# Kernel tuning notes

Measured on AMD Instinct MI355X. Metric: run time of the kernel, lower is better.

Reference implementation:

```python
import jax, jax.numpy as jnp
import numpy as np

D_MODEL = 1024
N_HEADS = 16
DEPTH = D_MODEL // N_HEADS
DFF = 4096
B, S = 2, 2048
EPS = 1e-6


def layer_norm(x, gamma, beta):
    m = jnp.mean(x, axis=-1, keepdims=True)
    v = jnp.mean(jnp.square(x - m), axis=-1, keepdims=True)
    return (x - m) * jax.lax.rsqrt(v + EPS) * gamma + beta


def setup_inputs() -> dict:
    key = jax.random.key(0)
    ks = jax.random.split(key, 16)
    s = 0.02
    x = jax.random.normal(ks[0], (B, S, D_MODEL), dtype=jnp.float32)
    # causal mask: 1.0 where attention is NOT allowed (upper triangle)
    mask = (1.0 - jnp.tril(jnp.ones((S, S), dtype=jnp.float32)))[None, None, :, :]
    return {
        "x": x,
        "mask": mask,
        "wq": jax.random.normal(ks[1], (D_MODEL, D_MODEL), jnp.float32) * s,
        "bq": jnp.zeros((D_MODEL,), jnp.float32),
        "wk": jax.random.normal(ks[2], (D_MODEL, D_MODEL), jnp.float32) * s,
        "bk": jnp.zeros((D_MODEL,), jnp.float32),
        "wv": jax.random.normal(ks[3], (D_MODEL, D_MODEL), jnp.float32) * s,
        "bv": jnp.zeros((D_MODEL,), jnp.float32),
        "wo": jax.random.normal(ks[4], (D_MODEL, D_MODEL), jnp.float32) * s,
        "bo": jnp.zeros((D_MODEL,), jnp.float32),
        "g1": jnp.ones((D_MODEL,), jnp.float32),
        "be1": jnp.zeros((D_MODEL,), jnp.float32),
        "w1": jax.random.normal(ks[5], (D_MODEL, DFF), jnp.float32) * s,
        "b1": jnp.zeros((DFF,), jnp.float32),
        "w2": jax.random.normal(ks[6], (DFF, D_MODEL), jnp.float32) * s,
        "b2": jnp.zeros((D_MODEL,), jnp.float32),
        "g2": jnp.ones((D_MODEL,), jnp.float32),
        "be2": jnp.zeros((D_MODEL,), jnp.float32),
    }


def reference(x, mask, wq, bq, wk, bk, wv, bv, wo, bo, g1, be1, w1, b1, w2, b2, g2, be2):
    b, s = x.shape[0], x.shape[1]

    def heads(t):  # [B,S,D_MODEL] -> [B,H,S,depth]
        return t.reshape(b, s, N_HEADS, DEPTH).transpose(0, 2, 1, 3)

    q = heads(x @ wq + bq)
    k = heads(x @ wk + bk)
    v = heads(x @ wv + bv)

    # [B,H,S,S] scores, materialized as in the original
    logits = jnp.einsum("bhqd,bhkd->bhqk", q, k) / jnp.sqrt(jnp.float32(DEPTH))
    logits = logits + mask * (-1e9)
    attn = jax.nn.softmax(logits, axis=-1)
    ctx = jnp.einsum("bhqk,bhkd->bhqd", attn, v)
    ctx = ctx.transpose(0, 2, 1, 3).reshape(b, s, D_MODEL)
    attn_out = ctx @ wo + bo

    out1 = layer_norm(x + attn_out, g1, be1)
    ffn = jax.nn.relu(out1 @ w1 + b1) @ w2 + b2
    out2 = layer_norm(out1 + ffn, g2, be2)
    return out2  # dropout inactive (training=False)
```

## Files before the change

### kernel.cpp

```cpp
#include <hip/hip_runtime.h>
#include <stdint.h>

typedef unsigned short u16;
typedef unsigned int u32;
typedef __attribute__((ext_vector_type(8))) short short8;
typedef __attribute__((ext_vector_type(4))) float f32x4;

#define NHEADS 16
#define SEQ 2048
#define DM 1024
#define MROWS 4096
#define FF 4096

static_assert(sizeof(short8) == 16, "short8 must be 16B");

__device__ __forceinline__ u16 f2b(float f) {
  u32 u = __float_as_uint(f);
  u += 0x7fffu + ((u >> 16) & 1u);
  return (u16)(u >> 16);
}
__device__ __forceinline__ u32 f2b2(float lo, float hi) {
  u32 a = __float_as_uint(lo); a += 0x7fffu + ((a >> 16) & 1u);
  u32 b = __float_as_uint(hi); b += 0x7fffu + ((b >> 16) & 1u);
  return (a >> 16) | (b & 0xffff0000u);
}
__device__ __forceinline__ u32 f2b2t(float lo, float hi) {
  return __builtin_amdgcn_perm(__float_as_uint(hi), __float_as_uint(lo), 0x07060302u);
}
__device__ __forceinline__ float b2f(u16 h) { return __uint_as_float(((u32)h) << 16); }

__device__ __forceinline__ void async_cp16(const u16* g, u16* l) {
  __builtin_amdgcn_global_load_lds((const __attribute__((address_space(1))) void*)g,
                                   (__attribute__((address_space(3))) void*)l, 16, 0, 0);
}

__global__ __launch_bounds__(256) void prep_k(const float* __restrict__ x,
                                              const float* __restrict__ wq,
                                              const float* __restrict__ wk,
                                              const float* __restrict__ wv,
                                              const float* __restrict__ wo,
                                              const float* __restrict__ w1,
                                              const float* __restrict__ w2,
                                              u16* __restrict__ xb, u16* __restrict__ btq,
                                              u16* __restrict__ wot, u16* __restrict__ w1t,
                                              u16* __restrict__ w2t) {
  const int bid = blockIdx.x, tid = threadIdx.x;
  if (bid < 4096) {
    const int i = bid * 256 + tid;
    const float4 v = ((const float4*)x)[i];
    uint2 o; o.x = f2b2(v.x, v.y); o.y = f2b2(v.z, v.w);
    ((uint2*)xb)[i] = o;
    return;
  }
  __shared__ float tile[32][33];
  const int tb = bid - 4096;
  const float* in; u16* out; int N, K, n0, k0;
  if (tb < 4096) {
    const int m = tb >> 10, t = tb & 1023;
    if (m == 0) { in = wq; out = btq; }
    else if (m == 1) { in = wk; out = btq + 1024 * 1024; }
    else if (m == 2) { in = wv; out = btq + 2 * 1024 * 1024; }
    else { in = wo; out = wot; }
    N = 1024; K = 1024; n0 = (t & 31) * 32; k0 = (t >> 5) * 32;
  } else if (tb < 8192) {
    const int t = tb - 4096;
    in = w1; out = w1t; N = 4096; K = 1024; n0 = (t & 127) * 32; k0 = (t >> 7) * 32;
  } else {
    const int t = tb - 8192;
    in = w2; out = w2t; N = 1024; K = 4096; n0 = (t & 31) * 32; k0 = (t >> 5) * 32;
  }
  const int tx = tid & 31, ty = tid >> 5;
#pragma unroll
  for (int i = 0; i < 4; i++) {
    const int r = ty + i * 8;
    tile[r][tx] = in[(long)(k0 + r) * N + n0 + tx];
  }
  __syncthreads();
#pragma unroll
  for (int i = 0; i < 4; i++) {
    const int r = ty + i * 8;
    out[(long)(n0 + r) * K + k0 + tx] = f2b(tile[tx][r]);
  }
}

#define BM 128
#define BN 128
#define BK 64
#define EPI_QKV 0
#define EPI_ADDRES 1
#define EPI_RELUB 2

template <int EPI>
__global__ __launch_bounds__(256, 2) void gemm_bt(
    const u16* __restrict__ A, const u16* __restrict__ Bt, const int M, const int N,
    const int K, const float* __restrict__ bias0, const float* __restrict__ bias1,
    const float* __restrict__ bias2, const float* __restrict__ resid,
    float* __restrict__ outF, u16* __restrict__ outB, u16* __restrict__ outQ,
    u16* __restrict__ outK, u16* __restrict__ outV) {
  __shared__ u16 As[BM * BK];
  __shared__ u16 Bs[BN * BK];
  const int tid = threadIdx.x;
  const int lane = tid & 63;
  const int wv = tid >> 6;
  const int quad = lane >> 4;
  const int lm = lane & 15;
  const int tn = blockIdx.x * BN;
  const int tm = blockIdx.y * BM;
  const int wr = (wv >> 1) * 64;
  const int wc = (wv & 1) * 64;
  const int wslotbase = tid & ~63;

  const f32x4 z4 = {0.f, 0.f, 0.f, 0.f};
  f32x4 acc[4][4];
#pragma unroll
  for (int i = 0; i < 4; i++)
#pragma unroll
    for (int j = 0; j < 4; j++) acc[i][j] = z4;

  for (int kk = 0; kk < K; kk += BK) {
    __syncthreads();
#pragma unroll
    for (int t = 0; t < 4; t++) {
      const int slot = t * 256 + tid;
      const int row = slot >> 3;
      const int c = (slot & 7) ^ (row & 7);
      async_cp16(A + (long)(tm + row) * K + kk + c * 8,
                 As + (long)(t * 256 + wslotbase) * 8);
    }
#pragma unroll
    for (int t = 0; t < 4; t++) {
      const int slot = t * 256 + tid;
      const int row = slot >> 3;
      const int c = (slot & 7) ^ (row & 7);
      async_cp16(Bt + (long)(tn + row) * K + kk + c * 8,
                 Bs + (long)(t * 256 + wslotbase) * 8);
    }
    __syncthreads();
#pragma unroll
    for (int ks = 0; ks < 2; ks++) {
      short8 af[4], bf[4];
#pragma unroll
      for (int mi = 0; mi < 4; mi++) {
        const int row = wr + mi * 16 + lm;
        const int cc = (4 * ks + quad) ^ (row & 7);
        af[mi] = *(const short8*)(As + row * 64 + cc * 8);
      }
#pragma unroll
      for (int ni = 0; ni < 4; ni++) {
        const int row = wc + ni * 16 + lm;
        const int cc = (4 * ks + quad) ^ (row & 7);
        bf[ni] = *(const short8*)(Bs + row * 64 + cc * 8);
      }
#pragma unroll
      for (int mi = 0; mi < 4; mi++)
#pragma unroll
        for (int ni = 0; ni < 4; ni++)
          acc[mi][ni] =
              __builtin_amdgcn_mfma_f32_16x16x32_bf16(af[mi], bf[ni], acc[mi][ni], 0, 0, 0);
    }
  }

  if constexpr (EPI == EPI_QKV) {
    const int which = tn >> 10;
    const int bb = tm >> 11;
    if (which < 2) {
      const float* bs = which == 0 ? bias0 : bias1;
      u16* os = which == 0 ? outQ : outK;
      const float scale = which == 0 ? 0.125f * 1.44269504f : 1.0f;
#pragma unroll
      for (int ni = 0; ni < 4; ni++) {
        const int n = tn + wc + ni * 16 + lm;
        const int hd = n & 1023;
        const int h = hd >> 6, dep = hd & 63;
        const float bval = bs[hd];
#pragma unroll
        for (int mi = 0; mi < 4; mi++) {
#pragma unroll
          for (int r = 0; r < 4; r++) {
            const int ss = (tm & 2047) + wr + mi * 16 + quad * 4 + r;
            os[(((long)(bb * NHEADS + h) * SEQ + ss) << 6) + dep] =
                f2b((acc[mi][ni][r] + bval) * scale);
          }
        }
      }
    } else {
#pragma unroll
      for (int ni = 0; ni < 4; ni++) {
        const int n = tn + wc + ni * 16 + lm;
        const int hd = n & 1023;
        const int h = hd >> 6, dep = hd & 63;
        const float bval = bias2[hd];
        u16* vrow = outV + ((long)(bb * NHEADS + h) * 64 + dep) * SEQ;
#pragma unroll
        for (int mi = 0; mi < 4; mi++) {
          const int ss = (tm & 2047) + wr + mi * 16 + quad * 4;
          uint2 o;
          o.x = f2b2(acc[mi][ni][0] + bval, acc[mi][ni][1] + bval);
          o.y = f2b2(acc[mi][ni][2] + bval, acc[mi][ni][3] + bval);
          *(uint2*)(vrow + ss) = o;
        }
      }
    }
  } else {
#pragma unroll
    for (int mi = 0; mi < 4; mi++) {
#pragma unroll
      for (int r = 0; r < 4; r++) {
        const int m = tm + wr + mi * 16 + quad * 4 + r;
        const long rowo = (long)m * N;
#pragma unroll
        for (int ni = 0; ni < 4; ni++) {
          const int n = tn + wc + ni * 16 + lm;
          const float v = acc[mi][ni][r] + bias0[n];
          if constexpr (EPI == EPI_ADDRES) {
            outF[rowo + n] = v + resid[rowo + n];
          } else {
            outB[rowo + n] = f2b(fmaxf(v, 0.f));
          }
        }
      }
    }
  }
}

__global__ __launch_bounds__(256, 3) void attn_fused(const u16* __restrict__ Q,
                                                     const u16* __restrict__ K,
                                                     const u16* __restrict__ Vt,
                                                     u16* __restrict__ O,
                                                     float* __restrict__ part,
                                                     float* __restrict__ lpart) {
  __shared__ u16 Ks[2][64 * 64];
  __shared__ u16 Vs[2][64 * 64];
  __shared__ u16 Ps[4][16 * 72];
  const int tid = threadIdx.x;
  const int lane = tid & 63, w = tid >> 6, quad = lane >> 4, lm = lane & 15;
  const int bid = blockIdx.x;
  const int idx = bid >> 5, hb = bid & 31;
  const int h = hb & 15, b = hb >> 4;
  int qt, c0, nkl, half;
  if (idx < 32) {
    qt = 16 + (idx >> 1);
    const int nk = qt + 1;
    const int h0 = (nk + 1) >> 1;
    half = idx & 1;
    if (half == 0) { c0 = 0; nkl = h0; } else { c0 = h0; nkl = nk - h0; }
  } else {
    qt = 47 - idx; c0 = 0; nkl = qt + 1; half = -1;
  }
  const long bh = (long)(b * NHEADS + h);
  const u16* Qb = Q + bh * SEQ * 64;
  const u16* Kb = K + bh * SEQ * 64;
  const u16* Vb = Vt + bh * (long)64 * SEQ;
  const int rbase = qt * 64 + w * 16;
  const int wslot = tid & ~63;

  long kgo[2], vgo[2];
  int ldso[2];
#pragma unroll
  for (int i = 0; i < 2; i++) {
    const int slot = i * 256 + tid;
    const int row = slot >> 3;
    const int cg = (slot & 7) ^ (row & 7);
    kgo[i] = (long)row * 64 + cg * 8;
    vgo[i] = (long)row * SEQ + cg * 8;
    ldso[i] = (i * 256 + wslot) * 8;
  }

  short8 qf[2];
#pragma unroll
  for (int ks = 0; ks < 2; ks++)
    qf[ks] = *(const short8*)(Qb + (long)(rbase + lm) * 64 + ks * 32 + quad * 8);

  const f32x4 z4 = {0.f, 0.f, 0.f, 0.f};
  f32x4 ctx[4];
#pragma unroll
  for (int d = 0; d < 4; d++) ctx[d] = z4;
  float lacc = 0.f;
  u16* myP = (u16*)Ps[w];

  {
    const long ko = (long)c0 * 64 * 64;
#pragma unroll
    for (int i = 0; i < 2; i++) {
      async_cp16(Kb + ko + kgo[i], Ks[0] + ldso[i]);
      async_cp16(Vb + c0 * 64 + vgo[i], Vs[0] + ldso[i]);
    }
  }

  for (int t = 0; t < nkl; t++) {
    const int cur = t & 1;
    const int k0 = (c0 + t) * 64;
    __syncthreads();
    if (t + 1 < nkl) {
      const long ko = (long)(k0 + 64) * 64;
#pragma unroll
      for (int i = 0; i < 2; i++) {
        async_cp16(Kb + ko + kgo[i], Ks[1 - cur] + ldso[i]);
        async_cp16(Vb + (k0 + 64) + vgo[i], Vs[1 - cur] + ldso[i]);
      }
    }
    const u16* Kc = Ks[cur];
    const u16* Vc = Vs[cur];
    short8 kf[4][2];
#pragma unroll
    for (int ni = 0; ni < 4; ni++) {
      const int row = ni * 16 + lm;
      const int r8 = row & 7;
#pragma unroll
      for (int ks = 0; ks < 2; ks++) {
        const int cc = (ks * 4 + quad) ^ r8;
        kf[ni][ks] = *(const short8*)(Kc + row * 64 + cc * 8);
      }
    }
    f32x4 sa[4];
#pragma unroll
    for (int i = 0; i < 4; i++) sa[i] = z4;
#pragma unroll
    for (int ks = 0; ks < 2; ks++)
#pragma unroll
      for (int ni = 0; ni < 4; ni++)
        sa[ni] = __builtin_amdgcn_mfma_f32_16x16x32_bf16(kf[ni][ks], qf[ks], sa[ni], 0, 0, 0);
    const int qrow = rbase + lm;
    if (k0 + 63 > rbase) {
#pragma unroll
      for (int ni = 0; ni < 4; ni++)
#pragma unroll
        for (int r = 0; r < 4; r++)
          if (k0 + ni * 16 + quad * 4 + r > qrow) sa[ni][r] = -1e9f;
    }
    float tsum = 0.f;
#pragma unroll
    for (int ni = 0; ni < 4; ni++) {
      const float p0 = exp2f(sa[ni][0]);
      const float p1 = exp2f(sa[ni][1]);
      const float p2 = exp2f(sa[ni][2]);
      const float p3 = exp2f(sa[ni][3]);
      tsum += (p0 + p1) + (p2 + p3);
      uint2 o; o.x = f2b2t(p0, p1); o.y = f2b2t(p2, p3);
      *(uint2*)(myP + lm * 72 + ni * 16 + quad * 4) = o;
    }
    lacc += tsum;
#pragma unroll
    for (int kc = 0; kc < 2; kc++) {
      const short8 bp = *(const short8*)(myP + lm * 72 + kc * 32 + quad * 8);
#pragma unroll
      for (int dni = 0; dni < 4; dni++) {
        const int row = dni * 16 + lm;
        const int cc = (kc * 4 + quad) ^ (row & 7);
        const short8 vfr = *(const short8*)(Vc + row * 64 + cc * 8);
        ctx[dni] = __builtin_amdgcn_mfma_f32_16x16x32_bf16(vfr, bp, ctx[dni], 0, 0, 0);
      }
    }
  }
  float l = lacc;
  l += __shfl_xor(l, 16);
  l += __shfl_xor(l, 32);
  if (half < 0) {
    const float inv = 1.0f / l;
    const int s = rbase + lm;
    const long base = (long)(b * SEQ + s) * DM + h * 64;
#pragma unroll
    for (int dni = 0; dni < 4; dni++) {
      uint2 o;
      o.x = f2b2(ctx[dni][0] * inv, ctx[dni][1] * inv);
      o.y = f2b2(ctx[dni][2] * inv, ctx[dni][3] * inv);
      *(uint2*)(O + base + dni * 16 + quad * 4) = o;
    }
  } else {
    const long pt = ((long)(hb * 16 + (qt - 16))) * 2 + half;
    float* po = part + pt * 4096 + (w * 16 + lm) * 64;
#pragma unroll
    for (int dni = 0; dni < 4; dni++)
      *(float4*)(po + dni * 16 + quad * 4) =
          make_float4(ctx[dni][0], ctx[dni][1], ctx[dni][2], ctx[dni][3]);
    if (quad == 0) lpart[pt * 64 + w * 16 + lm] = l;
  }
}

__global__ __launch_bounds__(256) void attn_combine(const float* __restrict__ part,
                                                    const float* __restrict__ lpart,
                                                    u16* __restrict__ O) {
  const int g = blockIdx.x;
  const int hb = g >> 4, qtr = g & 15;
  const int h = hb & 15, b = hb >> 4;
  const int qt = 16 + qtr;
  const long pt0 = ((long)(hb * 16 + qtr)) * 2;
  const float* p0 = part + pt0 * 4096;
  const float* p1 = p0 + 4096;
  const float* lp = lpart + pt0 * 64;
  const int tid = threadIdx.x;
  const int row = tid >> 2, d0 = (tid & 3) * 16;
  const float inv = 1.0f / (lp[row] + lp[64 + row]);
  const long off = (long)(b * SEQ + qt * 64 + row) * DM + h * 64 + d0;
  u32 o[8];
#pragma unroll
  for (int i = 0; i < 4; i++) {
    const float4 a = *(const float4*)(p0 + row * 64 + d0 + i * 4);
    const float4 c = *(const float4*)(p1 + row * 64 + d0 + i * 4);
    o[i * 2 + 0] = f2b2((a.x + c.x) * inv, (a.y + c.y) * inv);
    o[i * 2 + 1] = f2b2((a.z + c.z) * inv, (a.w + c.w) * inv);
  }
  *(uint4*)(O + off) = make_uint4(o[0], o[1], o[2], o[3]);
  *(uint4*)(O + off + 8) = make_uint4(o[4], o[5], o[6], o[7]);
}

template <bool WB>
__global__ __launch_bounds__(256) void ln_k(const float* __restrict__ in,
                                            const float* __restrict__ gam,
                                            const float* __restrict__ bet,
                                            float* __restrict__ outF,
                                            u16* __restrict__ outB) {
  __shared__ float red[8];
  const int row = blockIdx.x, tid = threadIdx.x;
  const long off = (long)row * DM;
  const float4 v = ((const float4*)(in + off))[tid];
  float s1 = v.x + v.y + v.z + v.w;
  float s2 = v.x * v.x + v.y * v.y + v.z * v.z + v.w * v.w;
  s1 += __shfl_xor(s1, 1); s2 += __shfl_xor(s2, 1);
  s1 += __shfl_xor(s1, 2); s2 += __shfl_xor(s2, 2);
  s1 += __shfl_xor(s1, 4); s2 += __shfl_xor(s2, 4);
  s1 += __shfl_xor(s1, 8); s2 += __shfl_xor(s2, 8);
  s1 += __shfl_xor(s1, 16); s2 += __shfl_xor(s2, 16);
  s1 += __shfl_xor(s1, 32); s2 += __shfl_xor(s2, 32);
  if ((tid & 63) == 0) { red[tid >> 6] = s1; red[4 + (tid >> 6)] = s2; }
  __syncthreads();
  const float mean = (red[0] + red[1] + red[2] + red[3]) * (1.f / DM);
  const float ex2 = (red[4] + red[5] + red[6] + red[7]) * (1.f / DM);
  const float var = fmaxf(ex2 - mean * mean, 0.f);
  const float rs = rsqrtf(var + 1e-6f);
  const float4 g4 = ((const float4*)gam)[tid];
  const float4 be4 = ((const float4*)bet)[tid];
  const float o0 = (v.x - mean) * rs * g4.x + be4.x;
  const float o1 = (v.y - mean) * rs * g4.y + be4.y;
  const float o2 = (v.z - mean) * rs * g4.z + be4.z;
  const float o3 = (v.w - mean) * rs * g4.w + be4.w;
  ((float4*)(outF + off))[tid] = make_float4(o0, o1, o2, o3);
  if constexpr (WB) {
    uint2 o; o.x = f2b2(o0, o1); o.y = f2b2(o2, o3);
    ((uint2*)(outB + off))[tid] = o;
  }
}

extern "C" void kernel_launch(void* const* d_in, const int* in_sizes, int n_in,
                              void* d_out, int out_size, void* d_ws, size_t ws_size,
                              hipStream_t stream) {
  (void)in_sizes; (void)n_in; (void)out_size; (void)ws_size;
  const float* x = (const float*)d_in[0];
  const float* wq = (const float*)d_in[2];
  const float* bq = (const float*)d_in[3];
  const float* wk = (const float*)d_in[4];
  const float* bk = (const float*)d_in[5];
  const float* wv = (const float*)d_in[6];
  const float* bv = (const float*)d_in[7];
  const float* wo = (const float*)d_in[8];
  const float* bo = (const float*)d_in[9];
  const float* g1 = (const float*)d_in[10];
  const float* be1 = (const float*)d_in[11];
  const float* w1 = (const float*)d_in[12];
  const float* b1 = (const float*)d_in[13];
  const float* w2 = (const float*)d_in[14];
  const float* b2 = (const float*)d_in[15];
  const float* g2 = (const float*)d_in[16];
  const float* be2 = (const float*)d_in[17];
  float* out = (float*)d_out;
  uint8_t* ws = (uint8_t*)d_ws;
  const size_t MB = 1024ull * 1024ull;
  u16* wot = (u16*)(ws + 0 * MB);
  u16* w1t = (u16*)(ws + 2 * MB);
  u16* w2t = (u16*)(ws + 10 * MB);
  u16* btq = (u16*)(ws + 18 * MB);
  u16* xb  = (u16*)(ws + 24 * MB);
  u16* qb  = (u16*)(ws + 32 * MB);
  u16* kb  = (u16*)(ws + 40 * MB);
  u16* vt  = (u16*)(ws + 48 * MB);
  u16* ctxb = (u16*)(ws + 56 * MB);
  float* apart = (float*)(ws + 64 * MB);
  float* lpart = (float*)(ws + 81 * MB);
  float* res1 = (float*)(ws + 88 * MB);
  u16* o1b = (u16*)(ws + 104 * MB);
  float* o1f = (float*)(ws + 112 * MB);
  u16* h1 = (u16*)(ws + 18 * MB);
  float* res2 = (float*)(ws + 88 * MB);

  prep_k<<<dim3(16384), dim3(256), 0, stream>>>(x, wq, wk, wv, wo, w1, w2, xb, btq, wot,
                                                w1t, w2t);

  gemm_bt<EPI_QKV><<<dim3(24, 32), dim3(256), 0, stream>>>(
      xb, btq, MROWS, 3072, 1024, bq, bk, bv, nullptr, nullptr, nullptr, qb, kb, vt);

  attn_fused<<<dim3(1536), dim3(256), 0, stream>>>(qb, kb, vt, ctxb, apart, lpart);
  attn_combine<<<dim3(512), dim3(256), 0, stream>>>(apart, lpart, ctxb);

  gemm_bt<EPI_ADDRES><<<dim3(8, 32), dim3(256), 0, stream>>>(
      ctxb, wot, MROWS, 1024, 1024, bo, nullptr, nullptr, x, res1, nullptr, nullptr,
      nullptr, nullptr);

  ln_k<true><<<dim3(4096), dim3(256), 0, stream>>>(res1, g1, be1, o1f, o1b);

  gemm_bt<EPI_RELUB><<<dim3(32, 32), dim3(256), 0, stream>>>(
      o1b, w1t, MROWS, 4096, 1024, b1, nullptr, nullptr, nullptr, nullptr, h1, nullptr,
      nullptr, nullptr);

  gemm_bt<EPI_ADDRES><<<dim3(8, 32), dim3(256), 0, stream>>>(
      h1, w2t, MROWS, 1024, 4096, b2, nullptr, nullptr, o1f, res2, nullptr, nullptr,
      nullptr, nullptr);

  ln_k<false><<<dim3(4096), dim3(256), 0, stream>>>(res2, g2, be2, out, nullptr);
}
```

Measured before the change: 359.8 us.

## Split-K the N=1024 GEMMs and fold bias/residual reduction into layernorm

```diff
diff --git a/kernel.cpp b/kernel.cpp
--- a/kernel.cpp
+++ b/kernel.cpp
@@ -87,14 +87,15 @@
 #define BN 128
 #define BK 64
 #define EPI_QKV 0
-#define EPI_ADDRES 1
 #define EPI_RELUB 2
+#define EPI_PART 3
 
 template <int EPI>
 __global__ __launch_bounds__(256, 2) void gemm_bt(
     const u16* __restrict__ A, const u16* __restrict__ Bt, const int M, const int N,
-    const int K, const float* __restrict__ bias0, const float* __restrict__ bias1,
-    const float* __restrict__ bias2, const float* __restrict__ resid,
+    const int KITER, const int LDA, const int KOFF,
+    const float* __restrict__ bias0, const float* __restrict__ bias1,
+    const float* __restrict__ bias2,
     float* __restrict__ outF, u16* __restrict__ outB, u16* __restrict__ outQ,
     u16* __restrict__ outK, u16* __restrict__ outV) {
   __shared__ u16 As[BM * BK];
@@ -104,11 +105,16 @@
   const int wv = tid >> 6;
   const int quad = lane >> 4;
   const int lm = lane & 15;
-  const int tn = blockIdx.x * BN;
-  const int tm = blockIdx.y * BM;
+  const int lid = blockIdx.y * gridDim.x + blockIdx.x;
+  const int s = lid >> 3;
+  const int tm = ((lid & 7) * 4 + (s & 3)) * BM;
+  const int tn = (s >> 2) * BN;
   const int wr = (wv >> 1) * 64;
   const int wc = (wv & 1) * 64;
   const int wslotbase = tid & ~63;
+  const long zoff = (long)blockIdx.z * KOFF;
+  const u16* Ap = A + zoff;
+  const u16* Btp = Bt + zoff;
 
   const f32x4 z4 = {0.f, 0.f, 0.f, 0.f};
   f32x4 acc[4][4];
@@ -117,14 +123,14 @@
 #pragma unroll
     for (int j = 0; j < 4; j++) acc[i][j] = z4;
 
-  for (int kk = 0; kk < K; kk += BK) {
+  for (int kk = 0; kk < KITER; kk += BK) {
     __syncthreads();
 #pragma unroll
     for (int t = 0; t < 4; t++) {
       const int slot = t * 256 + tid;
       const int row = slot >> 3;
       const int c = (slot & 7) ^ (row & 7);
-      async_cp16(A + (long)(tm + row) * K + kk + c * 8,
+      async_cp16(Ap + (long)(tm + row) * LDA + kk + c * 8,
                  As + (long)(t * 256 + wslotbase) * 8);
     }
 #pragma unroll
@@ -132,7 +138,7 @@
       const int slot = t * 256 + tid;
       const int row = slot >> 3;
       const int c = (slot & 7) ^ (row & 7);
-      async_cp16(Bt + (long)(tn + row) * K + kk + c * 8,
+      async_cp16(Btp + (long)(tn + row) * LDA + kk + c * 8,
                  Bs + (long)(t * 256 + wslotbase) * 8);
     }
     __syncthreads();
@@ -201,7 +207,8 @@
         }
       }
     }
-  } else {
+  } else if constexpr (EPI == EPI_PART) {
+    float* po = outF + (long)blockIdx.z * M * N;
 #pragma unroll
     for (int mi = 0; mi < 4; mi++) {
 #pragma unroll
@@ -211,12 +218,22 @@
 #pragma unroll
         for (int ni = 0; ni < 4; ni++) {
           const int n = tn + wc + ni * 16 + lm;
+          po[rowo + n] = acc[mi][ni][r];
+        }
+      }
+    }
+  } else {
+#pragma unroll
+    for (int mi = 0; mi < 4; mi++) {
+#pragma unroll
+      for (int r = 0; r < 4; r++) {
+        const int m = tm + wr + mi * 16 + quad * 4 + r;
+        const long rowo = (long)m * N;
+#pragma unroll
+        for (int ni = 0; ni < 4; ni++) {
+          const int n = tn + wc + ni * 16 + lm;
           const float v = acc[mi][ni][r] + bias0[n];
-          if constexpr (EPI == EPI_ADDRES) {
-            outF[rowo + n] = v + resid[rowo + n];
-          } else {
-            outB[rowo + n] = f2b(fmaxf(v, 0.f));
-          }
+          outB[rowo + n] = f2b(fmaxf(v, 0.f));
         }
       }
     }
@@ -405,15 +422,26 @@
 }
 
 template <bool WB>
-__global__ __launch_bounds__(256) void ln_k(const float* __restrict__ in,
-                                            const float* __restrict__ gam,
-                                            const float* __restrict__ bet,
-                                            float* __restrict__ outF,
-                                            u16* __restrict__ outB) {
+__global__ __launch_bounds__(256) void layernorm2_k(const float* __restrict__ p0,
+                                                    const float* __restrict__ p1,
+                                                    const float* __restrict__ resid,
+                                                    const float* __restrict__ bias,
+                                                    const float* __restrict__ gam,
+                                                    const float* __restrict__ bet,
+                                                    float* __restrict__ outF,
+                                                    u16* __restrict__ outB) {
   __shared__ float red[8];
   const int row = blockIdx.x, tid = threadIdx.x;
   const long off = (long)row * DM;
-  const float4 v = ((const float4*)(in + off))[tid];
+  const float4 a4 = ((const float4*)(p0 + off))[tid];
+  const float4 b4v = ((const float4*)(p1 + off))[tid];
+  const float4 r4 = ((const float4*)(resid + off))[tid];
+  const float4 bi4 = ((const float4*)bias)[tid];
+  float4 v;
+  v.x = a4.x + b4v.x + r4.x + bi4.x;
+  v.y = a4.y + b4v.y + r4.y + bi4.y;
+  v.z = a4.z + b4v.z + r4.z + bi4.z;
+  v.w = a4.w + b4v.w + r4.w + bi4.w;
   float s1 = v.x + v.y + v.z + v.w;
   float s2 = v.x * v.x + v.y * v.y + v.z * v.z + v.w * v.w;
   s1 += __shfl_xor(s1, 1); s2 += __shfl_xor(s2, 1);
@@ -476,34 +504,35 @@
   u16* ctxb = (u16*)(ws + 56 * MB);
   float* apart = (float*)(ws + 64 * MB);
   float* lpart = (float*)(ws + 81 * MB);
-  float* res1 = (float*)(ws + 88 * MB);
-  u16* o1b = (u16*)(ws + 104 * MB);
-  float* o1f = (float*)(ws + 112 * MB);
+  float* part = (float*)(ws + 64 * MB);
+  u16* o1b = (u16*)(ws + 96 * MB);
+  float* o1f = (float*)(ws + 104 * MB);
   u16* h1 = (u16*)(ws + 18 * MB);
-  float* res2 = (float*)(ws + 88 * MB);
 
   prep_k<<<dim3(16384), dim3(256), 0, stream>>>(x, wq, wk, wv, wo, w1, w2, xb, btq, wot,
                                                 w1t, w2t);
 
   gemm_bt<EPI_QKV><<<dim3(24, 32), dim3(256), 0, stream>>>(
-      xb, btq, MROWS, 3072, 1024, bq, bk, bv, nullptr, nullptr, nullptr, qb, kb, vt);
+      xb, btq, MROWS, 3072, 1024, 1024, 0, bq, bk, bv, nullptr, nullptr, qb, kb, vt);
 
   attn_fused<<<dim3(1536), dim3(256), 0, stream>>>(qb, kb, vt, ctxb, apart, lpart);
   attn_combine<<<dim3(512), dim3(256), 0, stream>>>(apart, lpart, ctxb);
 
-  gemm_bt<EPI_ADDRES><<<dim3(8, 32), dim3(256), 0, stream>>>(
-      ctxb, wot, MROWS, 1024, 1024, bo, nullptr, nullptr, x, res1, nullptr, nullptr,
+  gemm_bt<EPI_PART><<<dim3(8, 32, 2), dim3(256), 0, stream>>>(
+      ctxb, wot, MROWS, 1024, 512, 1024, 512, nullptr, nullptr, nullptr, part, nullptr,
+      nullptr, nullptr, nullptr);
+
+  layernorm2_k<true><<<dim3(4096), dim3(256), 0, stream>>>(
+      part, part + (long)MROWS * DM, x, bo, g1, be1, o1f, o1b);
+
+  gemm_bt<EPI_RELUB><<<dim3(32, 32), dim3(256), 0, stream>>>(
+      o1b, w1t, MROWS, 4096, 1024, 1024, 0, b1, nullptr, nullptr, nullptr, h1, nullptr,
       nullptr, nullptr);
 
-  ln_k<true><<<dim3(4096), dim3(256), 0, stream>>>(res1, g1, be1, o1f, o1b);
-
-  gemm_bt<EPI_RELUB><<<dim3(32, 32), dim3(256), 0, stream>>>(
-      o1b, w1t, MROWS, 4096, 1024, b1, nullptr, nullptr, nullptr, nullptr, h1, nullptr,
-      nullptr, nullptr);
-
-  gemm_bt<EPI_ADDRES><<<dim3(8, 32), dim3(256), 0, stream>>>(
-      h1, w2t, MROWS, 1024, 4096, b2, nullptr, nullptr, o1f, res2, nullptr, nullptr,
-      nullptr, nullptr);
-
-  ln_k<false><<<dim3(4096), dim3(256), 0, stream>>>(res2, g2, be2, out, nullptr);
-}
+  gemm_bt<EPI_PART><<<dim3(8, 32, 2), dim3(256), 0, stream>>>(
+      h1, w2t, MROWS, 1024, 2048, 4096, 2048, nullptr, nullptr, nullptr, part, nullptr,
+      nullptr, nullptr, nullptr);
+
+  layernorm2_k<false><<<dim3(4096), dim3(256), 0, stream>>>(
+      part, part + (long)MROWS * DM, o1f, b2, g2, be2, out, nullptr);
+}
```

New measurement: 346.8 us. 3.6% less time.
